# Kernel optimization log

Hardware: AMD Instinct MI355X
Metric: run time of the kernel (lower is better)

The kernel has to match this reference:

```python
import jax, jax.numpy as jnp
import numpy as np

D_MODEL = 4096
HIDDEN = 16384
N_TOKENS = 4096


def dequant4(packed, scales):
    """Unpack 4-bit signed values (2 per byte, high nibble first) and apply per-row scales.
    packed: [d_out, d_in//2] ints in [0,256); scales: [d_out, 1].
    Returns [d_out, d_in] float weights."""
    hi = (packed >> 4) - 8          # even columns
    lo = (packed & 15) - 8          # odd columns
    d_out = packed.shape[0]
    w = jnp.stack([hi, lo], axis=-1).reshape(d_out, -1).astype(scales.dtype)
    return w * scales


def setup_inputs() -> dict:
    key = jax.random.key(0)
    k1, k2, k3, k4, k5 = jax.random.split(key, 5)
    x = jax.random.normal(k1, (N_TOKENS, D_MODEL), dtype=jnp.float32)
    fc1_packed = jax.random.randint(k2, (HIDDEN, D_MODEL // 2), 0, 256, dtype=jnp.int32)
    fc1_scales = jax.random.uniform(k3, (HIDDEN, 1), dtype=jnp.float32) * 0.02 + 1e-4
    fc2_packed = jax.random.randint(k4, (D_MODEL, HIDDEN // 2), 0, 256, dtype=jnp.int32)
    fc2_scales = jax.random.uniform(k5, (D_MODEL, 1), dtype=jnp.float32) * 0.02 + 1e-4
    return {"x": x, "fc1_packed": fc1_packed, "fc1_scales": fc1_scales,
            "fc2_packed": fc2_packed, "fc2_scales": fc2_scales}


def reference(x, fc1_packed, fc1_scales, fc2_packed, fc2_scales):
    W1 = dequant4(fc1_packed, fc1_scales)   # [HIDDEN, D_MODEL]
    W2 = dequant4(fc2_packed, fc2_scales)   # [D_MODEL, HIDDEN]
    h = jax.nn.gelu(x @ W1.T)                # [N, HIDDEN]
    return h @ W2.T                          # [N, D_MODEL]
```

## Files before the change

kernel.cpp:

```cpp
#include <hip/hip_runtime.h>
#include <cstdint>

typedef unsigned short u16;
typedef unsigned int   u32;

#define D_MODEL 4096
#define HIDDEN  16384
#define NTOK    4096

typedef short bf16x8  __attribute__((ext_vector_type(8)));
typedef float floatx4 __attribute__((ext_vector_type(4)));

typedef __attribute__((address_space(1))) u32 gu32;
typedef __attribute__((address_space(3))) u32 lu32;

__device__ __forceinline__ void gl_lds16(const void* g, void* l) {
  __builtin_amdgcn_global_load_lds((gu32*)g, (lu32*)l, 16, 0, 0);
}

__device__ __forceinline__ u16 f32_bf16_rne(float f) {
  union { float f; u32 u; } c; c.f = f;
  u32 u = c.u;
  return (u16)((u + 0x7FFFu + ((u >> 16) & 1u)) >> 16);
}

__device__ __forceinline__ u32 cvt_pk_bf16(float lo, float hi) {
  u32 r;
  asm("v_cvt_pk_bf16_f32 %0, %1, %2" : "=v"(r) : "v"(lo), "v"(hi));
  return r;
}

__device__ __forceinline__ float gelu_tanh(float x) {
  float inner = 0.7978845608028654f * fmaf(0.044715f * x * x, x, x);
  float e  = __expf(2.0f * inner);
  float th = 1.0f - 2.0f / (e + 1.0f);
  return 0.5f * x * (1.0f + th);
}

__global__ void __launch_bounds__(256) cvt_f32_bf16(const float4* __restrict__ in,
                                                    ushort4* __restrict__ out) {
  int i = blockIdx.x * 256 + threadIdx.x;
  float4 v = in[i];
  ushort4 o;
  o.x = f32_bf16_rne(v.x);
  o.y = f32_bf16_rne(v.y);
  o.z = f32_bf16_rne(v.z);
  o.w = f32_bf16_rne(v.w);
  out[i] = o;
}

__global__ void __launch_bounds__(256)
repack_nib(const int4* __restrict__ in, uint4* __restrict__ out) {
  const size_t i = (size_t)blockIdx.x * 256 + threadIdx.x;
  int4 a = in[4 * i + 0], b = in[4 * i + 1], c = in[4 * i + 2], d = in[4 * i + 3];
  uint4 o;
  o.x = (u32)(a.x & 255) | ((u32)(a.y & 255) << 8) | ((u32)(a.z & 255) << 16) | ((u32)(a.w & 255) << 24);
  o.y = (u32)(b.x & 255) | ((u32)(b.y & 255) << 8) | ((u32)(b.z & 255) << 16) | ((u32)(b.w & 255) << 24);
  o.z = (u32)(c.x & 255) | ((u32)(c.y & 255) << 8) | ((u32)(c.z & 255) << 16) | ((u32)(c.w & 255) << 24);
  o.w = (u32)(d.x & 255) | ((u32)(d.y & 255) << 8) | ((u32)(d.z & 255) << 16) | ((u32)(d.w & 255) << 24);
  out[i] = o;
}

__device__ __forceinline__ void wr8(char* d, u32 v, float s, float m8s) {
  u32 b0 = v & 0xFFu, b1 = (v >> 8) & 0xFFu, b2 = (v >> 16) & 0xFFu, b3 = v >> 24;
  uint4 q;
  q.x = cvt_pk_bf16(fmaf((float)(b0 >> 4), s, m8s), fmaf((float)(b0 & 15u), s, m8s));
  q.y = cvt_pk_bf16(fmaf((float)(b1 >> 4), s, m8s), fmaf((float)(b1 & 15u), s, m8s));
  q.z = cvt_pk_bf16(fmaf((float)(b2 >> 4), s, m8s), fmaf((float)(b2 & 15u), s, m8s));
  q.w = cvt_pk_bf16(fmaf((float)(b3 >> 4), s, m8s), fmaf((float)(b3 & 15u), s, m8s));
  *(uint4*)d = q;
}


#define VMW(N) asm volatile("s_waitcnt vmcnt(" #N ")" ::: "memory")
#define FEN()  asm volatile("" ::: "memory")

#define ASTG(T, SEG)                                                           \
  do {                                                                         \
    const size_t kof_ = (size_t)(T) * 64 + (size_t)(((SEG) >> 1) * 32);        \
    char* d_ = ldsw + (((T) & 1) << 16) + ((SEG) << 14) + (w2 << 10);          \
    gl_lds16(ast0 + kof_, d_);                                                 \
    gl_lds16(ast1 + kof_, d_ + 1024);                                          \
  } while (0)

#define BLOAD(T, DST)                                                          \
  do {                                                                         \
    DST.x = bn0[(T) * 8];                                                      \
    DST.y = bn0[(T) * 8 + 4];                                                  \
    DST.z = bn1[(T) * 8];                                                      \
    DST.w = bn1[(T) * 8 + 4];                                                  \
  } while (0)

#define BDEQ(T, KS, V0, V1)                                                    \
  do {                                                                         \
    char* d_ = ldsw + (((T) & 1) << 16) + ((1 + 2 * (KS)) << 14) +             \
               (w2 << 10) + lane * 16;                                         \
    wr8(d_, (V0), s0, m8s0);                                                   \
    wr8(d_ + 1024, (V1), s1, m8s1);                                            \
  } while (0)

#define PH(BB, MH, S, RDB, STG)                                                \
  do {                                                                         \
    const char* ab_ = ldsr + ((BB) << 16) + ((S) * 32768);                     \
    _Pragma("unroll")                                                          \
    for (int f_ = 0; f_ < 4; ++f_)                                             \
      af[f_] = *(const bf16x8*)(ab_ + ((MH) * 4 + f_) * 1024 + aoff);          \
    if (RDB) {                                                                 \
      _Pragma("unroll")                                                        \
      for (int f_ = 0; f_ < 4; ++f_)                                           \
        bf[f_] = *(const bf16x8*)(ab_ + 16384 + f_ * 1024 + boff);             \
    }                                                                          \
    STG;                                                                       \
    __builtin_amdgcn_s_barrier();                                              \
    asm volatile("s_waitcnt lgkmcnt(0)" ::: "memory");                         \
    __builtin_amdgcn_sched_barrier(0);                                         \
    __builtin_amdgcn_s_setprio(1);                                             \
    _Pragma("unroll")                                                          \
    for (int f_ = 0; f_ < 4; ++f_) {                                           \
      _Pragma("unroll")                                                        \
      for (int n_ = 0; n_ < 4; ++n_)                                           \
        acc[(MH) * 4 + f_][n_] = __builtin_amdgcn_mfma_f32_16x16x32_bf16(      \
            af[f_], bf[n_], acc[(MH) * 4 + f_][n_], 0, 0, 0);                  \
    }                                                                          \
    __builtin_amdgcn_s_setprio(0);                                             \
    __builtin_amdgcn_s_barrier();                                              \
  } while (0)

template <int K, int N, bool GELU>
__global__ void __launch_bounds__(512, 2)
gemm_nt8(const u16* __restrict__ A, const u32* __restrict__ Bnib,
         const float* __restrict__ Bsc, u16* __restrict__ Cb,
         float* __restrict__ Cf) {
  __shared__ __align__(16) u16 lds[2 * 4 * 8192];
  char* ldsw = (char*)lds;
  const char* ldsr = (const char*)lds;

  const int tid  = threadIdx.x;
  const int lane = tid & 63;
  const int wave = tid >> 6;
  const int quad = lane >> 4;
  const int l16  = lane & 15;
  const int wm   = wave >> 2;
  const int wn   = wave & 3;

  const int gx  = gridDim.x;
  const int nwg = gx * gridDim.y;
  const int orig = blockIdx.y * gx + blockIdx.x;
  const int q = nwg >> 3, r = nwg & 7;
  const int xcd = orig & 7, lid = orig >> 3;
  const int wgid = (xcd < r ? xcd * (q + 1) : r * (q + 1) + (xcd - r) * q) + lid;
  const int n0 = (wgid % gx) * 256;
  const int m0 = (wgid / gx) * 256;

  const int w2   = wave * 2;
  const int rl   = lane >> 2;
  const int kcol = ((lane & 3) * 8) ^ ((lane & 32) ? 16 : 0);
  const u16* ast0 = A + (size_t)(m0 + w2 * 16 + rl) * K + kcol;
  const u16* ast1 = ast0 + (size_t)16 * K;

  const int brow0 = n0 + w2 * 16 + rl;
  const u32* bn0 = Bnib + (size_t)brow0 * (K / 8) + (kcol >> 3);
  const u32* bn1 = Bnib + (size_t)(brow0 + 16) * (K / 8) + (kcol >> 3);
  const float s0 = Bsc[brow0];
  const float s1 = Bsc[brow0 + 16];
  const float m8s0 = -8.0f * s0;
  const float m8s1 = -8.0f * s1;

  u32 pa = (u32)((wm * 128 + l16) * 64 + quad * 16);
  const u32 aoff = pa ^ (((pa >> 9) & 1) << 5);
  u32 pb = (u32)((wn * 64 + l16) * 64 + quad * 16);
  const u32 boff = pb ^ (((pb >> 9) & 1) << 5);

  floatx4 acc[8][4];
#pragma unroll
  for (int i = 0; i < 8; ++i)
#pragma unroll
    for (int j = 0; j < 4; ++j) acc[i][j] = (floatx4){0.f, 0.f, 0.f, 0.f};

  bf16x8 af[4], bf[4];
  uint4 bt0, bt1, bq0, bq1, bq0n, bq1n;

  ASTG(0, 0); ASTG(0, 2); ASTG(1, 0);
  BLOAD(0, bt0); BLOAD(1, bt1); BLOAD(2, bq0); BLOAD(3, bq1);
  FEN();
  VMW(8);
  BDEQ(0, 0, bt0.x, bt0.z);
  BDEQ(0, 1, bt0.y, bt0.w);
  BDEQ(1, 0, bt1.x, bt1.z);
  BDEQ(1, 1, bt1.y, bt1.w);
  asm volatile("s_waitcnt lgkmcnt(0)" ::: "memory");
  __builtin_amdgcn_s_barrier();

  const int KT = K / 64;
  for (int t = 0; t < KT - 4; t += 2) {
    PH(0, 0, 0, 1, ASTG(t + 1, 2); BLOAD(t + 4, bq0n); FEN());
    PH(0, 1, 0, 0, VMW(8); BDEQ(t + 2, 0, bq0.x, bq0.z));
    PH(0, 1, 1, 1, ASTG(t + 2, 0); FEN());
    PH(0, 0, 1, 0, VMW(8); BDEQ(t + 2, 1, bq0.y, bq0.w));
    PH(1, 0, 0, 1, ASTG(t + 2, 2); BLOAD(t + 5, bq1n); FEN());
    PH(1, 1, 0, 0, VMW(8); BDEQ(t + 3, 0, bq1.x, bq1.z));
    PH(1, 1, 1, 1, ASTG(t + 3, 0); FEN());
    PH(1, 0, 1, 0, VMW(8); BDEQ(t + 3, 1, bq1.y, bq1.w));
    bq0 = bq0n;
    bq1 = bq1n;
  }
  {
    const int t = KT - 4;
    PH(0, 0, 0, 1, ASTG(t + 1, 2); FEN());
    PH(0, 1, 0, 0, VMW(8); BDEQ(t + 2, 0, bq0.x, bq0.z));
    PH(0, 1, 1, 1, ASTG(t + 2, 0); FEN());
    PH(0, 0, 1, 0, VMW(4); BDEQ(t + 2, 1, bq0.y, bq0.w));
    PH(1, 0, 0, 1, ASTG(t + 2, 2); FEN());
    PH(1, 1, 0, 0, VMW(4); BDEQ(t + 3, 0, bq1.x, bq1.z));
    PH(1, 1, 1, 1, ASTG(t + 3, 0); FEN());
    PH(1, 0, 1, 0, VMW(4); BDEQ(t + 3, 1, bq1.y, bq1.w));
  }
  {
    const int t = KT - 2;
    PH(0, 0, 0, 1, ASTG(t + 1, 2); FEN());
    PH(0, 1, 0, 0, VMW(4));
    PH(0, 1, 1, 1, (void)0);
    PH(0, 0, 1, 0, VMW(2));
    PH(1, 0, 0, 1, VMW(0));
    PH(1, 1, 0, 0, (void)0);
    PH(1, 1, 1, 1, (void)0);
    PH(1, 0, 1, 0, (void)0);
  }

  const int crow0 = m0 + wm * 128 + quad * 4;
  const int ccol0 = n0 + wn * 64 + l16;
#pragma unroll
  for (int mf = 0; mf < 8; ++mf) {
#pragma unroll
    for (int rr = 0; rr < 4; ++rr) {
      const size_t row = (size_t)(crow0 + mf * 16 + rr);
#pragma unroll
      for (int nf = 0; nf < 4; ++nf) {
        float v = acc[mf][nf][rr];
        const size_t idx = row * N + (size_t)(ccol0 + nf * 16);
        if constexpr (GELU) {
          Cb[idx] = f32_bf16_rne(gelu_tanh(v));
        } else {
          Cf[idx] = v;
        }
      }
    }
  }
}

#undef PH
#undef BDEQ
#undef BLOAD
#undef ASTG
#undef VMW
#undef FEN

template <int K, int N, bool GELU>
__global__ void __launch_bounds__(256)
gemm_dq(const u16* __restrict__ A, const int* __restrict__ Bp,
        const float* __restrict__ Bsc, u16* __restrict__ Cb, float* __restrict__ Cf) {
  __shared__ __align__(16) u16 As[128 * 32];
  __shared__ __align__(16) u16 Bs[128 * 32];

  const int tid  = threadIdx.x;
  const int lane = tid & 63;
  const int wave = tid >> 6;
  const int quad = lane >> 4;
  const int l16  = lane & 15;
  const int wm = wave >> 1, wn = wave & 1;

  const int n0 = blockIdx.x * 128;
  const int m0 = blockIdx.y * 128;

  const int brow  = tid >> 1;
  const int bhalf = tid & 1;
  const float s   = Bsc[n0 + brow];
  const float m8s = -8.0f * s;
  const int4* bp  = (const int4*)(Bp + (size_t)(n0 + brow) * (K / 2)) + bhalf * 2;
  u16* blds = Bs + (brow >> 4) * 512 + (2 * bhalf) * 128 + (brow & 15) * 8;

  const u16* ag = A + (size_t)(m0 + l16) * K + (size_t)quad * 8;
  u16* alds0 = As + (wave * 2 + 0) * 512;
  u16* alds1 = As + (wave * 2 + 1) * 512;

  floatx4 acc[4][4];
#pragma unroll
  for (int i = 0; i < 4; ++i)
#pragma unroll
    for (int j = 0; j < 4; ++j)
      acc[i][j] = (floatx4){0.f, 0.f, 0.f, 0.f};

  const int KT = K / 32;
  for (int kt = 0; kt < KT; ++kt) {
    int4 w0 = bp[(size_t)kt * 4 + 0];
    int4 w1 = bp[(size_t)kt * 4 + 1];
    __syncthreads();
    gl_lds16(ag + (size_t)(wave * 2 + 0) * 16 * K + kt * 32, alds0);
    gl_lds16(ag + (size_t)(wave * 2 + 1) * 16 * K + kt * 32, alds1);
    int wv[8] = {w0.x, w0.y, w0.z, w0.w, w1.x, w1.y, w1.z, w1.w};
    union { u16 e[16]; uint4 q[2]; } u;
#pragma unroll
    for (int j = 0; j < 8; ++j) {
      int v = wv[j];
      u.e[2 * j]     = f32_bf16_rne(fmaf((float)(v >> 4), s, m8s));
      u.e[2 * j + 1] = f32_bf16_rne(fmaf((float)(v & 15), s, m8s));
    }
    *(uint4*)(blds)       = u.q[0];
    *(uint4*)(blds + 128) = u.q[1];
    __syncthreads();

    bf16x8 af[4], bf[4];
#pragma unroll
    for (int im = 0; im < 4; ++im)
      af[im] = *(const bf16x8*)(As + (wm * 4 + im) * 512 + quad * 128 + l16 * 8);
#pragma unroll
    for (int in = 0; in < 4; ++in)
      bf[in] = *(const bf16x8*)(Bs + (wn * 4 + in) * 512 + quad * 128 + l16 * 8);
#pragma unroll
    for (int im = 0; im < 4; ++im)
#pragma unroll
      for (int in = 0; in < 4; ++in)
        acc[im][in] = __builtin_amdgcn_mfma_f32_16x16x32_bf16(af[im], bf[in], acc[im][in], 0, 0, 0);
  }

#pragma unroll
  for (int im = 0; im < 4; ++im) {
#pragma unroll
    for (int r = 0; r < 4; ++r) {
      const int row = m0 + wm * 64 + im * 16 + quad * 4 + r;
#pragma unroll
      for (int in = 0; in < 4; ++in) {
        const int col = n0 + wn * 64 + in * 16 + l16;
        float v = acc[im][in][r];
        if constexpr (GELU) {
          Cb[(size_t)row * N + col] = f32_bf16_rne(gelu_tanh(v));
        } else {
          Cf[(size_t)row * N + col] = v;
        }
      }
    }
  }
}

extern "C" void kernel_launch(void* const* d_in, const int* in_sizes, int n_in,
                              void* d_out, int out_size, void* d_ws, size_t ws_size,
                              hipStream_t stream) {
  const float* x   = (const float*)d_in[0];
  const int*   f1p = (const int*)d_in[1];
  const float* f1s = (const float*)d_in[2];
  const int*   f2p = (const int*)d_in[3];
  const float* f2s = (const float*)d_in[4];
  float* out = (float*)d_out;

  const size_t xb_bytes  = (size_t)NTOK * D_MODEL * 2;
  const size_t h_bytes   = (size_t)NTOK * HIDDEN * 2;
  const size_t nib_bytes = (size_t)HIDDEN * D_MODEL / 2;
  const size_t base      = xb_bytes + h_bytes;
  if (ws_size < base) return;

  u16* xb = (u16*)d_ws;
  u16* h  = xb + (size_t)NTOK * D_MODEL;

  cvt_f32_bf16<<<(NTOK * D_MODEL) / 1024, 256, 0, stream>>>((const float4*)x, (ushort4*)xb);

  if (ws_size < base + 2 * nib_bytes) {
    gemm_dq<D_MODEL, HIDDEN, true>
        <<<dim3(HIDDEN / 128, NTOK / 128), 256, 0, stream>>>(xb, f1p, f1s, h, nullptr);
    gemm_dq<HIDDEN, D_MODEL, false>
        <<<dim3(D_MODEL / 128, NTOK / 128), 256, 0, stream>>>(h, f2p, f2s, nullptr, out);
    return;
  }

  u32* nib1 = (u32*)(h + (size_t)NTOK * HIDDEN);
  u32* nib2 = nib1 + nib_bytes / 4;

  const int nblk = (int)((size_t)HIDDEN * (D_MODEL / 2) / 16 / 256);
  repack_nib<<<nblk, 256, 0, stream>>>((const int4*)f1p, (uint4*)nib1);
  repack_nib<<<nblk, 256, 0, stream>>>((const int4*)f2p, (uint4*)nib2);

  gemm_nt8<D_MODEL, HIDDEN, true>
      <<<dim3(HIDDEN / 256, NTOK / 256), 512, 0, stream>>>(xb, nib1, f1s, h, nullptr);
  gemm_nt8<HIDDEN, D_MODEL, false>
      <<<dim3(D_MODEL / 256, NTOK / 256), 512, 0, stream>>>(h, nib2, f2s, nullptr, out);
}
```

Baseline: 1.386 ms.

## Shrink GEMM tile to 128x256 with K=32 steps and deeper pipeline

Replaces the 256x256 tile with K-step 64 by a 128x256 tile with K-step 32. It uses a four-slot A ring buffer and a double-buffered dequantized-B buffer in a 64KB LDS allocation, and launch bounds allow four workgroups per CU. Accumulators drop from 8x4 to 4x4 fragments to cut register pressure and raise occupancy. In exchange, the larger grid dequantizes each B tile twice as often, and the smaller tile lowers A/B reuse per loaded byte.

```diff
diff --git a/kernel.cpp b/kernel.cpp
--- a/kernel.cpp
+++ b/kernel.cpp
@@ -75,41 +75,29 @@
 #define VMW(N) asm volatile("s_waitcnt vmcnt(" #N ")" ::: "memory")
 #define FEN()  asm volatile("" ::: "memory")
 
-#define ASTG(T, SEG)                                                           \
+#define ASTG(T) gl_lds16(ast0 + (size_t)(T) * 32, ldsw + (((T) & 3) << 13) + (wave << 10))
+
+#define BLOAD(T, Q)                                                            \
   do {                                                                         \
-    const size_t kof_ = (size_t)(T) * 64 + (size_t)(((SEG) >> 1) * 32);        \
-    char* d_ = ldsw + (((T) & 1) << 16) + ((SEG) << 14) + (w2 << 10);          \
-    gl_lds16(ast0 + kof_, d_);                                                 \
-    gl_lds16(ast1 + kof_, d_ + 1024);                                          \
+    Q.x = bn0[(T) * 4];                                                        \
+    Q.y = bn1[(T) * 4];                                                        \
   } while (0)
 
-#define BLOAD(T, DST)                                                          \
+#define BDEQ(T, Q)                                                             \
   do {                                                                         \
-    DST.x = bn0[(T) * 8];                                                      \
-    DST.y = bn0[(T) * 8 + 4];                                                  \
-    DST.z = bn1[(T) * 8];                                                      \
-    DST.w = bn1[(T) * 8 + 4];                                                  \
+    char* d_ = ldsw + 32768 + (((T) & 1) << 14) + (w2 << 10) + lane * 16;      \
+    wr8(d_, (Q).x, s0, m8s0);                                                  \
+    wr8(d_ + 1024, (Q).y, s1, m8s1);                                           \
   } while (0)
 
-#define BDEQ(T, KS, V0, V1)                                                    \
+#define PH(AB, BB, VME, STG)                                                   \
   do {                                                                         \
-    char* d_ = ldsw + (((T) & 1) << 16) + ((1 + 2 * (KS)) << 14) +             \
-               (w2 << 10) + lane * 16;                                         \
-    wr8(d_, (V0), s0, m8s0);                                                   \
-    wr8(d_ + 1024, (V1), s1, m8s1);                                            \
-  } while (0)
-
-#define PH(BB, MH, S, RDB, STG)                                                \
-  do {                                                                         \
-    const char* ab_ = ldsr + ((BB) << 16) + ((S) * 32768);                     \
     _Pragma("unroll")                                                          \
     for (int f_ = 0; f_ < 4; ++f_)                                             \
-      af[f_] = *(const bf16x8*)(ab_ + ((MH) * 4 + f_) * 1024 + aoff);          \
-    if (RDB) {                                                                 \
-      _Pragma("unroll")                                                        \
-      for (int f_ = 0; f_ < 4; ++f_)                                           \
-        bf[f_] = *(const bf16x8*)(ab_ + 16384 + f_ * 1024 + boff);             \
-    }                                                                          \
+      af[f_] = *(const bf16x8*)(ldsr + ((AB) << 13) + f_ * 1024 + aoff);       \
+    _Pragma("unroll")                                                          \
+    for (int f_ = 0; f_ < 4; ++f_)                                             \
+      bf[f_] = *(const bf16x8*)(ldsr + 32768 + ((BB) << 14) + f_ * 1024 + boff);\
     STG;                                                                       \
     __builtin_amdgcn_s_barrier();                                              \
     asm volatile("s_waitcnt lgkmcnt(0)" ::: "memory");                         \
@@ -119,19 +107,22 @@
     for (int f_ = 0; f_ < 4; ++f_) {                                           \
       _Pragma("unroll")                                                        \
       for (int n_ = 0; n_ < 4; ++n_)                                           \
-        acc[(MH) * 4 + f_][n_] = __builtin_amdgcn_mfma_f32_16x16x32_bf16(      \
-            af[f_], bf[n_], acc[(MH) * 4 + f_][n_], 0, 0, 0);                  \
+        acc[f_][n_] = __builtin_amdgcn_mfma_f32_16x16x32_bf16(                 \
+            af[f_], bf[n_], acc[f_][n_], 0, 0, 0);                             \
     }                                                                          \
     __builtin_amdgcn_s_setprio(0);                                             \
+    if ((VME) == 5) VMW(5);                                                    \
+    if ((VME) == 3) VMW(3);                                                    \
+    if ((VME) == 0) VMW(0);                                                    \
     __builtin_amdgcn_s_barrier();                                              \
   } while (0)
 
 template <int K, int N, bool GELU>
-__global__ void __launch_bounds__(512, 2)
-gemm_nt8(const u16* __restrict__ A, const u32* __restrict__ Bnib,
-         const float* __restrict__ Bsc, u16* __restrict__ Cb,
-         float* __restrict__ Cf) {
-  __shared__ __align__(16) u16 lds[2 * 4 * 8192];
+__global__ void __launch_bounds__(512, 4)
+gemm_f(const u16* __restrict__ A, const u32* __restrict__ Bnib,
+       const float* __restrict__ Bsc, u16* __restrict__ Cb,
+       float* __restrict__ Cf) {
+  __shared__ __align__(16) u16 lds[32768];
   char* ldsw = (char*)lds;
   const char* ldsr = (const char*)lds;
 
@@ -150,13 +141,12 @@
   const int xcd = orig & 7, lid = orig >> 3;
   const int wgid = (xcd < r ? xcd * (q + 1) : r * (q + 1) + (xcd - r) * q) + lid;
   const int n0 = (wgid % gx) * 256;
-  const int m0 = (wgid / gx) * 256;
+  const int m0 = (wgid / gx) * 128;
 
   const int w2   = wave * 2;
   const int rl   = lane >> 2;
   const int kcol = ((lane & 3) * 8) ^ ((lane & 32) ? 16 : 0);
-  const u16* ast0 = A + (size_t)(m0 + w2 * 16 + rl) * K + kcol;
-  const u16* ast1 = ast0 + (size_t)16 * K;
+  const u16* ast0 = A + (size_t)(m0 + wave * 16 + rl) * K + kcol;
 
   const int brow0 = n0 + w2 * 16 + rl;
   const u32* bn0 = Bnib + (size_t)brow0 * (K / 8) + (kcol >> 3);
@@ -166,71 +156,47 @@
   const float m8s0 = -8.0f * s0;
   const float m8s1 = -8.0f * s1;
 
-  u32 pa = (u32)((wm * 128 + l16) * 64 + quad * 16);
+  u32 pa = (u32)((wm * 64 + l16) * 64 + quad * 16);
   const u32 aoff = pa ^ (((pa >> 9) & 1) << 5);
   u32 pb = (u32)((wn * 64 + l16) * 64 + quad * 16);
   const u32 boff = pb ^ (((pb >> 9) & 1) << 5);
 
-  floatx4 acc[8][4];
-#pragma unroll
-  for (int i = 0; i < 8; ++i)
+  floatx4 acc[4][4];
+#pragma unroll
+  for (int i = 0; i < 4; ++i)
 #pragma unroll
     for (int j = 0; j < 4; ++j) acc[i][j] = (floatx4){0.f, 0.f, 0.f, 0.f};
 
   bf16x8 af[4], bf[4];
-  uint4 bt0, bt1, bq0, bq1, bq0n, bq1n;
-
-  ASTG(0, 0); ASTG(0, 2); ASTG(1, 0);
-  BLOAD(0, bt0); BLOAD(1, bt1); BLOAD(2, bq0); BLOAD(3, bq1);
+  uint2 q0, q1, q2, q3;
+
+  ASTG(0); ASTG(1);
+  BLOAD(0, q0); BLOAD(1, q1); BLOAD(2, q2);
   FEN();
-  VMW(8);
-  BDEQ(0, 0, bt0.x, bt0.z);
-  BDEQ(0, 1, bt0.y, bt0.w);
-  BDEQ(1, 0, bt1.x, bt1.z);
-  BDEQ(1, 1, bt1.y, bt1.w);
+  VMW(6);
+  BDEQ(0, q0);
   asm volatile("s_waitcnt lgkmcnt(0)" ::: "memory");
   __builtin_amdgcn_s_barrier();
 
-  const int KT = K / 64;
-  for (int t = 0; t < KT - 4; t += 2) {
-    PH(0, 0, 0, 1, ASTG(t + 1, 2); BLOAD(t + 4, bq0n); FEN());
-    PH(0, 1, 0, 0, VMW(8); BDEQ(t + 2, 0, bq0.x, bq0.z));
-    PH(0, 1, 1, 1, ASTG(t + 2, 0); FEN());
-    PH(0, 0, 1, 0, VMW(8); BDEQ(t + 2, 1, bq0.y, bq0.w));
-    PH(1, 0, 0, 1, ASTG(t + 2, 2); BLOAD(t + 5, bq1n); FEN());
-    PH(1, 1, 0, 0, VMW(8); BDEQ(t + 3, 0, bq1.x, bq1.z));
-    PH(1, 1, 1, 1, ASTG(t + 3, 0); FEN());
-    PH(1, 0, 1, 0, VMW(8); BDEQ(t + 3, 1, bq1.y, bq1.w));
-    bq0 = bq0n;
-    bq1 = bq1n;
+  const int KT = K / 32;
+  for (int u = 0; u < KT - 4; u += 4) {
+    PH(0, 0, 5, BDEQ(u + 1, q1); ASTG(u + 2); BLOAD(u + 3, q3); FEN());
+    PH(1, 1, 5, BDEQ(u + 2, q2); ASTG(u + 3); BLOAD(u + 4, q0); FEN());
+    PH(2, 0, 5, BDEQ(u + 3, q3); ASTG(u + 4); BLOAD(u + 5, q1); FEN());
+    PH(3, 1, 5, BDEQ(u + 4, q0); ASTG(u + 5); BLOAD(u + 6, q2); FEN());
   }
   {
-    const int t = KT - 4;
-    PH(0, 0, 0, 1, ASTG(t + 1, 2); FEN());
-    PH(0, 1, 0, 0, VMW(8); BDEQ(t + 2, 0, bq0.x, bq0.z));
-    PH(0, 1, 1, 1, ASTG(t + 2, 0); FEN());
-    PH(0, 0, 1, 0, VMW(4); BDEQ(t + 2, 1, bq0.y, bq0.w));
-    PH(1, 0, 0, 1, ASTG(t + 2, 2); FEN());
-    PH(1, 1, 0, 0, VMW(4); BDEQ(t + 3, 0, bq1.x, bq1.z));
-    PH(1, 1, 1, 1, ASTG(t + 3, 0); FEN());
-    PH(1, 0, 1, 0, VMW(4); BDEQ(t + 3, 1, bq1.y, bq1.w));
-  }
-  {
-    const int t = KT - 2;
-    PH(0, 0, 0, 1, ASTG(t + 1, 2); FEN());
-    PH(0, 1, 0, 0, VMW(4));
-    PH(0, 1, 1, 1, (void)0);
-    PH(0, 0, 1, 0, VMW(2));
-    PH(1, 0, 0, 1, VMW(0));
-    PH(1, 1, 0, 0, (void)0);
-    PH(1, 1, 1, 1, (void)0);
-    PH(1, 0, 1, 0, (void)0);
-  }
-
-  const int crow0 = m0 + wm * 128 + quad * 4;
+    const int u = KT - 4;
+    PH(0, 0, 5, BDEQ(u + 1, q1); ASTG(u + 2); BLOAD(u + 3, q3); FEN());
+    PH(1, 1, 3, BDEQ(u + 2, q2); ASTG(u + 3); FEN());
+    PH(2, 0, 0, BDEQ(u + 3, q3));
+    PH(3, 1, -1, (void)0);
+  }
+
+  const int crow0 = m0 + wm * 64 + quad * 4;
   const int ccol0 = n0 + wn * 64 + l16;
 #pragma unroll
-  for (int mf = 0; mf < 8; ++mf) {
+  for (int mf = 0; mf < 4; ++mf) {
 #pragma unroll
     for (int rr = 0; rr < 4; ++rr) {
       const size_t row = (size_t)(crow0 + mf * 16 + rr);
@@ -378,8 +344,8 @@
   repack_nib<<<nblk, 256, 0, stream>>>((const int4*)f1p, (uint4*)nib1);
   repack_nib<<<nblk, 256, 0, stream>>>((const int4*)f2p, (uint4*)nib2);
 
-  gemm_nt8<D_MODEL, HIDDEN, true>
-      <<<dim3(HIDDEN / 256, NTOK / 256), 512, 0, stream>>>(xb, nib1, f1s, h, nullptr);
-  gemm_nt8<HIDDEN, D_MODEL, false>
-      <<<dim3(D_MODEL / 256, NTOK / 256), 512, 0, stream>>>(h, nib2, f2s, nullptr, out);
-}
+  gemm_f<D_MODEL, HIDDEN, true>
+      <<<dim3(HIDDEN / 256, NTOK / 128), 512, 0, stream>>>(xb, nib1, f1s, h, nullptr);
+  gemm_f<HIDDEN, D_MODEL, false>
+      <<<dim3(D_MODEL / 256, NTOK / 128), 512, 0, stream>>>(h, nib2, f2s, nullptr, out);
+}
```

Result: slower. 3.131 ms (+125.9%).

## Switch GEMMs to fp16, dequantize nibbles with magic-number trick, defer scales to epilogue

Applied to the files above, without the earlier changes.

Changes activations and weights from bf16 to fp16 and uses fp16 MFMA. Nibble dequantization now uses the 0x6400 magic-exponent trick with a packed half add and byte permutes, not per-element float FMAs and conversions. The per-row weight scale is applied once to the accumulator in the epilogue rather than during dequant. The aim is to cut VALU work in the dequant path inside the pipelined GEMM. It also moves the B dequant writes after the MFMA block, adding an lgkmcnt wait, and risks fp16 overflow or precision differences in h.

```diff
diff --git a/kernel.cpp b/kernel.cpp
--- a/kernel.cpp
+++ b/kernel.cpp
@@ -8,8 +8,9 @@
 #define HIDDEN  16384
 #define NTOK    4096
 
-typedef short bf16x8  __attribute__((ext_vector_type(8)));
-typedef float floatx4 __attribute__((ext_vector_type(4)));
+typedef _Float16 f16x8 __attribute__((ext_vector_type(8)));
+typedef _Float16 h2    __attribute__((ext_vector_type(2)));
+typedef float floatx4  __attribute__((ext_vector_type(4)));
 
 typedef __attribute__((address_space(1))) u32 gu32;
 typedef __attribute__((address_space(3))) u32 lu32;
@@ -18,16 +19,9 @@
   __builtin_amdgcn_global_load_lds((gu32*)g, (lu32*)l, 16, 0, 0);
 }
 
-__device__ __forceinline__ u16 f32_bf16_rne(float f) {
-  union { float f; u32 u; } c; c.f = f;
-  u32 u = c.u;
-  return (u16)((u + 0x7FFFu + ((u >> 16) & 1u)) >> 16);
-}
-
-__device__ __forceinline__ u32 cvt_pk_bf16(float lo, float hi) {
-  u32 r;
-  asm("v_cvt_pk_bf16_f32 %0, %1, %2" : "=v"(r) : "v"(lo), "v"(hi));
-  return r;
+__device__ __forceinline__ u16 f32_f16(float f) {
+  _Float16 h = (_Float16)f;
+  return __builtin_bit_cast(u16, h);
 }
 
 __device__ __forceinline__ float gelu_tanh(float x) {
@@ -37,15 +31,15 @@
   return 0.5f * x * (1.0f + th);
 }
 
-__global__ void __launch_bounds__(256) cvt_f32_bf16(const float4* __restrict__ in,
-                                                    ushort4* __restrict__ out) {
+__global__ void __launch_bounds__(256) cvt_f32_f16(const float4* __restrict__ in,
+                                                   ushort4* __restrict__ out) {
   int i = blockIdx.x * 256 + threadIdx.x;
   float4 v = in[i];
   ushort4 o;
-  o.x = f32_bf16_rne(v.x);
-  o.y = f32_bf16_rne(v.y);
-  o.z = f32_bf16_rne(v.z);
-  o.w = f32_bf16_rne(v.w);
+  o.x = f32_f16(v.x);
+  o.y = f32_f16(v.y);
+  o.z = f32_f16(v.z);
+  o.w = f32_f16(v.w);
   out[i] = o;
 }
 
@@ -61,18 +55,24 @@
   out[i] = o;
 }
 
-__device__ __forceinline__ void wr8(char* d, u32 v, float s, float m8s) {
-  u32 b0 = v & 0xFFu, b1 = (v >> 8) & 0xFFu, b2 = (v >> 16) & 0xFFu, b3 = v >> 24;
+__device__ __forceinline__ void wr8i(char* d, u32 v) {
+  const u32 M = 0x000F000Fu, G = 0x64006400u;
+  const h2 C = __builtin_bit_cast(h2, 0xE408E408u);
+  u32 d0 = __builtin_bit_cast(u32, __builtin_bit_cast(h2, ((v >> 4) & M) | G) + C);
+  u32 d1 = __builtin_bit_cast(u32, __builtin_bit_cast(h2, (v & M) | G) + C);
+  u32 d2 = __builtin_bit_cast(u32, __builtin_bit_cast(h2, ((v >> 12) & M) | G) + C);
+  u32 d3 = __builtin_bit_cast(u32, __builtin_bit_cast(h2, ((v >> 8) & M) | G) + C);
   uint4 q;
-  q.x = cvt_pk_bf16(fmaf((float)(b0 >> 4), s, m8s), fmaf((float)(b0 & 15u), s, m8s));
-  q.y = cvt_pk_bf16(fmaf((float)(b1 >> 4), s, m8s), fmaf((float)(b1 & 15u), s, m8s));
-  q.z = cvt_pk_bf16(fmaf((float)(b2 >> 4), s, m8s), fmaf((float)(b2 & 15u), s, m8s));
-  q.w = cvt_pk_bf16(fmaf((float)(b3 >> 4), s, m8s), fmaf((float)(b3 & 15u), s, m8s));
+  q.x = __builtin_amdgcn_perm(d1, d0, 0x05040100u);
+  q.y = __builtin_amdgcn_perm(d3, d2, 0x05040100u);
+  q.z = __builtin_amdgcn_perm(d1, d0, 0x07060302u);
+  q.w = __builtin_amdgcn_perm(d3, d2, 0x07060302u);
   *(uint4*)d = q;
 }
 
 
 #define VMW(N) asm volatile("s_waitcnt vmcnt(" #N ")" ::: "memory")
+#define LGK0() asm volatile("s_waitcnt lgkmcnt(0)" ::: "memory")
 #define FEN()  asm volatile("" ::: "memory")
 
 #define ASTG(T, SEG)                                                           \
@@ -95,34 +95,35 @@
   do {                                                                         \
     char* d_ = ldsw + (((T) & 1) << 16) + ((1 + 2 * (KS)) << 14) +             \
                (w2 << 10) + lane * 16;                                         \
-    wr8(d_, (V0), s0, m8s0);                                                   \
-    wr8(d_ + 1024, (V1), s1, m8s1);                                            \
+    wr8i(d_, (V0));                                                            \
+    wr8i(d_ + 1024, (V1));                                                     \
   } while (0)
 
-#define PH(BB, MH, S, RDB, STG)                                                \
+#define PH(BB, MH, S, RDB, PRE, POST)                                          \
   do {                                                                         \
     const char* ab_ = ldsr + ((BB) << 16) + ((S) * 32768);                     \
     _Pragma("unroll")                                                          \
     for (int f_ = 0; f_ < 4; ++f_)                                             \
-      af[f_] = *(const bf16x8*)(ab_ + ((MH) * 4 + f_) * 1024 + aoff);          \
+      af[f_] = *(const f16x8*)(ab_ + ((MH) * 4 + f_) * 1024 + aoff);           \
     if (RDB) {                                                                 \
       _Pragma("unroll")                                                        \
       for (int f_ = 0; f_ < 4; ++f_)                                           \
-        bf[f_] = *(const bf16x8*)(ab_ + 16384 + f_ * 1024 + boff);             \
+        bf[f_] = *(const f16x8*)(ab_ + 16384 + f_ * 1024 + boff);              \
     }                                                                          \
-    STG;                                                                       \
+    PRE;                                                                       \
     __builtin_amdgcn_s_barrier();                                              \
-    asm volatile("s_waitcnt lgkmcnt(0)" ::: "memory");                         \
+    LGK0();                                                                    \
     __builtin_amdgcn_sched_barrier(0);                                         \
     __builtin_amdgcn_s_setprio(1);                                             \
     _Pragma("unroll")                                                          \
     for (int f_ = 0; f_ < 4; ++f_) {                                           \
       _Pragma("unroll")                                                        \
       for (int n_ = 0; n_ < 4; ++n_)                                           \
-        acc[(MH) * 4 + f_][n_] = __builtin_amdgcn_mfma_f32_16x16x32_bf16(      \
+        acc[(MH) * 4 + f_][n_] = __builtin_amdgcn_mfma_f32_16x16x32_f16(       \
             af[f_], bf[n_], acc[(MH) * 4 + f_][n_], 0, 0, 0);                  \
     }                                                                          \
     __builtin_amdgcn_s_setprio(0);                                             \
+    POST;                                                                      \
     __builtin_amdgcn_s_barrier();                                              \
   } while (0)
 
@@ -152,6 +153,11 @@
   const int n0 = (wgid % gx) * 256;
   const int m0 = (wgid / gx) * 256;
 
+  float scl[4];
+#pragma unroll
+  for (int nf = 0; nf < 4; ++nf) scl[nf] = Bsc[n0 + wn * 64 + nf * 16 + l16];
+  FEN();
+
   const int w2   = wave * 2;
   const int rl   = lane >> 2;
   const int kcol = ((lane & 3) * 8) ^ ((lane & 32) ? 16 : 0);
@@ -161,10 +167,6 @@
   const int brow0 = n0 + w2 * 16 + rl;
   const u32* bn0 = Bnib + (size_t)brow0 * (K / 8) + (kcol >> 3);
   const u32* bn1 = Bnib + (size_t)(brow0 + 16) * (K / 8) + (kcol >> 3);
-  const float s0 = Bsc[brow0];
-  const float s1 = Bsc[brow0 + 16];
-  const float m8s0 = -8.0f * s0;
-  const float m8s1 = -8.0f * s1;
 
   u32 pa = (u32)((wm * 128 + l16) * 64 + quad * 16);
   const u32 aoff = pa ^ (((pa >> 9) & 1) << 5);
@@ -177,7 +179,7 @@
 #pragma unroll
     for (int j = 0; j < 4; ++j) acc[i][j] = (floatx4){0.f, 0.f, 0.f, 0.f};
 
-  bf16x8 af[4], bf[4];
+  f16x8 af[4], bf[4];
   uint4 bt0, bt1, bq0, bq1, bq0n, bq1n;
 
   ASTG(0, 0); ASTG(0, 2); ASTG(1, 0);
@@ -188,43 +190,43 @@
   BDEQ(0, 1, bt0.y, bt0.w);
   BDEQ(1, 0, bt1.x, bt1.z);
   BDEQ(1, 1, bt1.y, bt1.w);
-  asm volatile("s_waitcnt lgkmcnt(0)" ::: "memory");
+  LGK0();
   __builtin_amdgcn_s_barrier();
 
   const int KT = K / 64;
   for (int t = 0; t < KT - 4; t += 2) {
-    PH(0, 0, 0, 1, ASTG(t + 1, 2); BLOAD(t + 4, bq0n); FEN());
-    PH(0, 1, 0, 0, VMW(8); BDEQ(t + 2, 0, bq0.x, bq0.z));
-    PH(0, 1, 1, 1, ASTG(t + 2, 0); FEN());
-    PH(0, 0, 1, 0, VMW(8); BDEQ(t + 2, 1, bq0.y, bq0.w));
-    PH(1, 0, 0, 1, ASTG(t + 2, 2); BLOAD(t + 5, bq1n); FEN());
-    PH(1, 1, 0, 0, VMW(8); BDEQ(t + 3, 0, bq1.x, bq1.z));
-    PH(1, 1, 1, 1, ASTG(t + 3, 0); FEN());
-    PH(1, 0, 1, 0, VMW(8); BDEQ(t + 3, 1, bq1.y, bq1.w));
+    PH(0, 0, 0, 1, ASTG(t + 1, 2); BLOAD(t + 4, bq0n); FEN(), (void)0);
+    PH(0, 1, 0, 0, (void)0,        VMW(8); BDEQ(t + 2, 0, bq0.x, bq0.z); LGK0());
+    PH(0, 1, 1, 1, ASTG(t + 2, 0); FEN(), (void)0);
+    PH(0, 0, 1, 0, (void)0,        VMW(8); BDEQ(t + 2, 1, bq0.y, bq0.w); LGK0());
+    PH(1, 0, 0, 1, ASTG(t + 2, 2); BLOAD(t + 5, bq1n); FEN(), (void)0);
+    PH(1, 1, 0, 0, (void)0,        VMW(8); BDEQ(t + 3, 0, bq1.x, bq1.z); LGK0());
+    PH(1, 1, 1, 1, ASTG(t + 3, 0); FEN(), (void)0);
+    PH(1, 0, 1, 0, (void)0,        VMW(8); BDEQ(t + 3, 1, bq1.y, bq1.w); LGK0());
     bq0 = bq0n;
     bq1 = bq1n;
   }
   {
     const int t = KT - 4;
-    PH(0, 0, 0, 1, ASTG(t + 1, 2); FEN());
-    PH(0, 1, 0, 0, VMW(8); BDEQ(t + 2, 0, bq0.x, bq0.z));
-    PH(0, 1, 1, 1, ASTG(t + 2, 0); FEN());
-    PH(0, 0, 1, 0, VMW(4); BDEQ(t + 2, 1, bq0.y, bq0.w));
-    PH(1, 0, 0, 1, ASTG(t + 2, 2); FEN());
-    PH(1, 1, 0, 0, VMW(4); BDEQ(t + 3, 0, bq1.x, bq1.z));
-    PH(1, 1, 1, 1, ASTG(t + 3, 0); FEN());
-    PH(1, 0, 1, 0, VMW(4); BDEQ(t + 3, 1, bq1.y, bq1.w));
+    PH(0, 0, 0, 1, ASTG(t + 1, 2); FEN(), (void)0);
+    PH(0, 1, 0, 0, (void)0, VMW(8); BDEQ(t + 2, 0, bq0.x, bq0.z); LGK0());
+    PH(0, 1, 1, 1, ASTG(t + 2, 0); FEN(), (void)0);
+    PH(0, 0, 1, 0, (void)0, VMW(4); BDEQ(t + 2, 1, bq0.y, bq0.w); LGK0());
+    PH(1, 0, 0, 1, ASTG(t + 2, 2); FEN(), (void)0);
+    PH(1, 1, 0, 0, (void)0, VMW(4); BDEQ(t + 3, 0, bq1.x, bq1.z); LGK0());
+    PH(1, 1, 1, 1, ASTG(t + 3, 0); FEN(), (void)0);
+    PH(1, 0, 1, 0, (void)0, VMW(4); BDEQ(t + 3, 1, bq1.y, bq1.w); LGK0());
   }
   {
     const int t = KT - 2;
-    PH(0, 0, 0, 1, ASTG(t + 1, 2); FEN());
-    PH(0, 1, 0, 0, VMW(4));
-    PH(0, 1, 1, 1, (void)0);
-    PH(0, 0, 1, 0, VMW(2));
-    PH(1, 0, 0, 1, VMW(0));
-    PH(1, 1, 0, 0, (void)0);
-    PH(1, 1, 1, 1, (void)0);
-    PH(1, 0, 1, 0, (void)0);
+    PH(0, 0, 0, 1, ASTG(t + 1, 2); FEN(), (void)0);
+    PH(0, 1, 0, 0, (void)0, VMW(4));
+    PH(0, 1, 1, 1, (void)0, (void)0);
+    PH(0, 0, 1, 0, (void)0, VMW(2));
+    PH(1, 0, 0, 1, (void)0, VMW(0));
+    PH(1, 1, 0, 0, (void)0, (void)0);
+    PH(1, 1, 1, 1, (void)0, (void)0);
+    PH(1, 0, 1, 0, (void)0, (void)0);
   }
 
   const int crow0 = m0 + wm * 128 + quad * 4;
@@ -236,10 +238,10 @@
       const size_t row = (size_t)(crow0 + mf * 16 + rr);
 #pragma unroll
       for (int nf = 0; nf < 4; ++nf) {
-        float v = acc[mf][nf][rr];
+        float v = acc[mf][nf][rr] * scl[nf];
         const size_t idx = row * N + (size_t)(ccol0 + nf * 16);
         if constexpr (GELU) {
-          Cb[idx] = f32_bf16_rne(gelu_tanh(v));
+          Cb[idx] = f32_f16(gelu_tanh(v));
         } else {
           Cf[idx] = v;
         }
@@ -253,6 +255,7 @@
 #undef BLOAD
 #undef ASTG
 #undef VMW
+#undef LGK0
 #undef FEN
 
 template <int K, int N, bool GELU>
@@ -302,25 +305,25 @@
 #pragma unroll
     for (int j = 0; j < 8; ++j) {
       int v = wv[j];
-      u.e[2 * j]     = f32_bf16_rne(fmaf((float)(v >> 4), s, m8s));
-      u.e[2 * j + 1] = f32_bf16_rne(fmaf((float)(v & 15), s, m8s));
+      u.e[2 * j]     = f32_f16(fmaf((float)(v >> 4), s, m8s));
+      u.e[2 * j + 1] = f32_f16(fmaf((float)(v & 15), s, m8s));
     }
     *(uint4*)(blds)       = u.q[0];
     *(uint4*)(blds + 128) = u.q[1];
     __syncthreads();
 
-    bf16x8 af[4], bf[4];
+    f16x8 af[4], bf[4];
 #pragma unroll
     for (int im = 0; im < 4; ++im)
-      af[im] = *(const bf16x8*)(As + (wm * 4 + im) * 512 + quad * 128 + l16 * 8);
+      af[im] = *(const f16x8*)(As + (wm * 4 + im) * 512 + quad * 128 + l16 * 8);
 #pragma unroll
     for (int in = 0; in < 4; ++in)
-      bf[in] = *(const bf16x8*)(Bs + (wn * 4 + in) * 512 + quad * 128 + l16 * 8);
+      bf[in] = *(const f16x8*)(Bs + (wn * 4 + in) * 512 + quad * 128 + l16 * 8);
 #pragma unroll
     for (int im = 0; im < 4; ++im)
 #pragma unroll
       for (int in = 0; in < 4; ++in)
-        acc[im][in] = __builtin_amdgcn_mfma_f32_16x16x32_bf16(af[im], bf[in], acc[im][in], 0, 0, 0);
+        acc[im][in] = __builtin_amdgcn_mfma_f32_16x16x32_f16(af[im], bf[in], acc[im][in], 0, 0, 0);
   }
 
 #pragma unroll
@@ -333,7 +336,7 @@
         const int col = n0 + wn * 64 + in * 16 + l16;
         float v = acc[im][in][r];
         if constexpr (GELU) {
-          Cb[(size_t)row * N + col] = f32_bf16_rne(gelu_tanh(v));
+          Cb[(size_t)row * N + col] = f32_f16(gelu_tanh(v));
         } else {
           Cf[(size_t)row * N + col] = v;
         }
@@ -361,7 +364,7 @@
   u16* xb = (u16*)d_ws;
   u16* h  = xb + (size_t)NTOK * D_MODEL;
 
-  cvt_f32_bf16<<<(NTOK * D_MODEL) / 1024, 256, 0, stream>>>((const float4*)x, (ushort4*)xb);
+  cvt_f32_f16<<<(NTOK * D_MODEL) / 1024, 256, 0, stream>>>((const float4*)x, (ushort4*)xb);
 
   if (ws_size < base + 2 * nib_bytes) {
     gemm_dq<D_MODEL, HIDDEN, true>
```

Measured after the change: 1.280 ms. 7.7% less time.
